# Kernel tuning notes

Hardware: AMD Instinct MI355X
Metric: run time of the kernel (lower is better)

The kernel has to match this reference:

```python
import jax, jax.numpy as jnp
import numpy as np

N, E, D_IN, D_OUT = 100000, 1600000, 128, 128
EPS = 1e-12  # torch F.normalize clamp


def setup_inputs() -> dict:
    key = jax.random.key(0)
    ks = jax.random.split(key, 8)
    return {
        "x": jax.random.normal(ks[0], (N, D_IN), dtype=jnp.float32),
        "edge_src": jax.random.randint(ks[1], (E,), 0, N, dtype=jnp.int32),
        "edge_dst": jax.random.randint(ks[2], (E,), 0, N, dtype=jnp.int32),
        "edge_weight": jax.random.uniform(ks[3], (E,), dtype=jnp.float32),
        "W_l": jax.random.normal(ks[4], (D_IN, D_OUT), dtype=jnp.float32) / np.sqrt(D_IN),
        "b_l": jax.random.normal(ks[5], (D_OUT,), dtype=jnp.float32) * 0.01,
        "W_r": jax.random.normal(ks[6], (D_IN, D_OUT), dtype=jnp.float32) / np.sqrt(D_IN),
        "b_r": jax.random.normal(ks[7], (D_OUT,), dtype=jnp.float32) * 0.01,
    }


def reference(x, edge_src, edge_dst, edge_weight, W_l, b_l, W_r, b_r):
    # spmm(adj, x): weighted gather of source node features, scatter-add to targets
    agg = jax.ops.segment_sum(x[edge_src] * edge_weight[:, None], edge_dst,
                              num_segments=x.shape[0])          # [N, D_IN]
    out = agg @ W_l + b_l + (x @ W_r + b_r)                      # lin_l + lin_r (num_tgt == N)
    # L1 normalize along features (F.normalize, p=1, dim=1)
    l1 = jnp.maximum(jnp.sum(jnp.abs(out), axis=1, keepdims=True), EPS)
    return out / l1
```

## Files before the change

kernel.cpp:

```cpp
#include <hip/hip_runtime.h>
#include <hip/hip_fp16.h>


static constexpr int D = 128;
static constexpr int NB = 1024;
static constexpr int CBITS = 7;
static constexpr int CSZ = 1 << CBITS;
static constexpr int NPART = 256;

typedef _Float16 half8 __attribute__((ext_vector_type(8)));
typedef float f32x4 __attribute__((ext_vector_type(4)));

__global__ __launch_bounds__(256) void cvt_x_fp16(
    const float4* __restrict__ x4, __half2* __restrict__ xh2, int n4)
{
    int i = blockIdx.x * blockDim.x + threadIdx.x;
    int stride = gridDim.x * blockDim.x;
    for (; i < n4; i += stride) {
        float4 v = x4[i];
        xh2[2 * i + 0] = __floats2half2_rn(v.x, v.y);
        xh2[2 * i + 1] = __floats2half2_rn(v.z, v.w);
    }
}

__global__ __launch_bounds__(256) void wt_build(
    const float* __restrict__ Wl, const float* __restrict__ Wr,
    __half* __restrict__ wt)
{
    const int idx = blockIdx.x * blockDim.x + threadIdx.x;
    if (idx >= 128 * 256) return;
    const int c = idx >> 8;
    const int k = idx & 255;
    const float v = (k < 128) ? Wl[(size_t)k * D + c] : Wr[(size_t)(k - 128) * D + c];
    wt[(size_t)c * 256 + k] = __float2half(v);
}

__global__ __launch_bounds__(256) void coarse_count(
    const int* __restrict__ edst, int* __restrict__ bhist, int E, int chunk)
{
    __shared__ int hist[NB];
    for (int t = threadIdx.x; t < NB; t += 256) hist[t] = 0;
    __syncthreads();
    const int beg = blockIdx.x * chunk;
    const int end = min(E, beg + chunk);
    for (int e = beg + threadIdx.x; e < end; e += 256)
        atomicAdd(&hist[edst[e] >> CBITS], 1);
    __syncthreads();
    for (int t = threadIdx.x; t < NB; t += 256)
        bhist[(size_t)blockIdx.x * NB + t] = hist[t];
}

__global__ __launch_bounds__(64) void bucket_scan(
    int* __restrict__ bhist, int* __restrict__ ctot)
{
    const int t = blockIdx.x * 64 + threadIdx.x;
    int run = 0;
    for (int b = 0; b < NPART; b += 8) {
        int v[8];
#pragma unroll
        for (int i = 0; i < 8; ++i)
            v[i] = bhist[(size_t)(b + i) * NB + t];
#pragma unroll
        for (int i = 0; i < 8; ++i) {
            const int c = v[i];
            bhist[(size_t)(b + i) * NB + t] = run;
            run += c;
        }
    }
    ctot[t] = run;
}

__global__ __launch_bounds__(NB) void coarse_scan(
    const int* __restrict__ ctot, int* __restrict__ cbase,
    int* __restrict__ offs, int N, int E)
{
    __shared__ int s[NB];
    const int t = threadIdx.x;
    const int v = ctot[t];
    s[t] = v;
    __syncthreads();
    for (int off = 1; off < NB; off <<= 1) {
        const int u = (t >= off) ? s[t - off] : 0;
        __syncthreads();
        s[t] += u;
        __syncthreads();
    }
    cbase[t] = s[t] - v;
    if (t == NB - 1) { cbase[NB] = s[t]; offs[N] = E; }
}

__global__ __launch_bounds__(256) void coarse_partition(
    const int* __restrict__ esrc, const int* __restrict__ edst,
    const float* __restrict__ ew, const int* __restrict__ bhist,
    const int* __restrict__ cbase,
    int2* __restrict__ cpairs, int E, int chunk)
{
    __shared__ int cur[NB];
    for (int t = threadIdx.x; t < NB; t += 256)
        cur[t] = bhist[(size_t)blockIdx.x * NB + t] + cbase[t];
    __syncthreads();
    const int beg = blockIdx.x * chunk;
    const int end = min(E, beg + chunk);
    for (int e = beg + threadIdx.x; e < end; e += 256) {
        const int d = edst[e];
        const int pos = atomicAdd(&cur[d >> CBITS], 1);
        cpairs[pos] = make_int2(((d & (CSZ - 1)) << 20) | esrc[e],
                                __float_as_int(ew[e]));
    }
}

__global__ __launch_bounds__(256) void fine_sort(
    const int2* __restrict__ cpairs, const int* __restrict__ cbase,
    int* __restrict__ offs, int2* __restrict__ pairs, int N)
{
    __shared__ int hist[CSZ];
    __shared__ int scn[CSZ];
    const int b = blockIdx.x;
    const int t = threadIdx.x;
    const int s0 = cbase[b], s1 = cbase[b + 1];
    if (t < CSZ) hist[t] = 0;
    __syncthreads();
    for (int i = s0 + t; i < s1; i += 256)
        atomicAdd(&hist[(cpairs[i].x >> 20) & (CSZ - 1)], 1);
    __syncthreads();
    if (t < CSZ) scn[t] = hist[t];
    __syncthreads();
    for (int off = 1; off < CSZ; off <<= 1) {
        int u = 0;
        if (t < CSZ && t >= off) u = scn[t - off];
        __syncthreads();
        if (t < CSZ) scn[t] += u;
        __syncthreads();
    }
    if (t < CSZ) {
        const int base = s0 + scn[t] - hist[t];
        const int node = (b << CBITS) + t;
        if (node < N) offs[node] = base;
        hist[t] = base;
    }
    __syncthreads();
    for (int i = s0 + t; i < s1; i += 256) {
        const int2 p = cpairs[i];
        const int pos = atomicAdd(&hist[(p.x >> 20) & (CSZ - 1)], 1);
        pairs[pos] = make_int2(p.x & 0xFFFFF, p.y);
    }
}

template <bool FP16X>
__global__ __launch_bounds__(256) void sage_gather(
    const void* __restrict__ xrows,
    const int2* __restrict__ pairs,
    const int* __restrict__ offs,
    void* __restrict__ agg,
    int N)
{
    int node = (blockIdx.x * blockDim.x + threadIdx.x) >> 6;
    const int lane = threadIdx.x & 63;
    if (node >= N) return;
    node = __builtin_amdgcn_readfirstlane(node);
    const int beg = offs[node];
    const int end = offs[node + 1];
    const int sub = lane >> 5;
    const int cl  = lane & 31;

    const __half* __restrict__ xh = (const __half*)xrows;
    const float*  __restrict__ xf = (const float*)xrows;

    float a0 = 0.f, a1 = 0.f, a2 = 0.f, a3 = 0.f;
    int k = beg;
    for (; k + 8 <= end; k += 8) {
        int s_[4]; float w_[4];
#pragma unroll
        for (int i = 0; i < 4; ++i) {
            const int2 ea = pairs[k + 2 * i + 0];
            const int2 eb = pairs[k + 2 * i + 1];
            s_[i] = sub ? eb.x : ea.x;
            w_[i] = __int_as_float(sub ? eb.y : ea.y);
        }
        if (FP16X) {
            float2 raw[4];
#pragma unroll
            for (int i = 0; i < 4; ++i)
                raw[i] = *reinterpret_cast<const float2*>(&xh[(size_t)s_[i] * D + cl * 4]);
#pragma unroll
            for (int i = 0; i < 4; ++i) {
                union { float2 f2; __half2 h[2]; } u;
                u.f2 = raw[i];
                const float2 f01 = __half22float2(u.h[0]);
                const float2 f23 = __half22float2(u.h[1]);
                a0 = fmaf(f01.x, w_[i], a0);
                a1 = fmaf(f01.y, w_[i], a1);
                a2 = fmaf(f23.x, w_[i], a2);
                a3 = fmaf(f23.y, w_[i], a3);
            }
        } else {
            float4 raw[4];
#pragma unroll
            for (int i = 0; i < 4; ++i)
                raw[i] = *reinterpret_cast<const float4*>(&xf[(size_t)s_[i] * D + cl * 4]);
#pragma unroll
            for (int i = 0; i < 4; ++i) {
                a0 = fmaf(raw[i].x, w_[i], a0);
                a1 = fmaf(raw[i].y, w_[i], a1);
                a2 = fmaf(raw[i].z, w_[i], a2);
                a3 = fmaf(raw[i].w, w_[i], a3);
            }
        }
    }
    for (int t = 0; k + t < end; ++t) {
        if (sub == (t & 1)) {
            const int2 p = pairs[k + t];
            const float w = __int_as_float(p.y);
            if (FP16X) {
                union { float2 f2; __half2 h[2]; } u;
                u.f2 = *reinterpret_cast<const float2*>(&xh[(size_t)p.x * D + cl * 4]);
                const float2 f01 = __half22float2(u.h[0]);
                const float2 f23 = __half22float2(u.h[1]);
                a0 = fmaf(f01.x, w, a0); a1 = fmaf(f01.y, w, a1);
                a2 = fmaf(f23.x, w, a2); a3 = fmaf(f23.y, w, a3);
            } else {
                const float4 v = *reinterpret_cast<const float4*>(&xf[(size_t)p.x * D + cl * 4]);
                a0 = fmaf(v.x, w, a0); a1 = fmaf(v.y, w, a1);
                a2 = fmaf(v.z, w, a2); a3 = fmaf(v.w, w, a3);
            }
        }
    }
    a0 += __shfl_xor(a0, 32, 64);
    a1 += __shfl_xor(a1, 32, 64);
    a2 += __shfl_xor(a2, 32, 64);
    a3 += __shfl_xor(a3, 32, 64);

    if (sub == 0) {
        if (FP16X) {
            union { __half2 h[2]; int2 i2; } u;
            u.h[0] = __floats2half2_rn(a0, a1);
            u.h[1] = __floats2half2_rn(a2, a3);
            *reinterpret_cast<int2*>(&((__half*)agg)[(size_t)node * D + cl * 4]) = u.i2;
        } else {
            *reinterpret_cast<float4*>(&((float*)agg)[(size_t)node * D + cl * 4]) =
                make_float4(a0, a1, a2, a3);
        }
    }
}

__global__ __launch_bounds__(256) void sage_scatter(
    const float* __restrict__ x,
    const int* __restrict__ esrc,
    const int* __restrict__ edst,
    const float* __restrict__ ew,
    float* agg, int E)
{
    const int lane = threadIdx.x & 63;
    const int warp = (blockIdx.x * blockDim.x + threadIdx.x) >> 6;
    const int nwarps = (gridDim.x * blockDim.x) >> 6;
    const float2* __restrict__ x2 = reinterpret_cast<const float2*>(x);
    for (int e = warp; e < E; e += nwarps) {
        const int s = esrc[e];
        const int d = edst[e];
        const float w = ew[e];
        const float2 xv = x2[s * 64 + lane];
        atomicAdd(&agg[d * D + lane * 2 + 0], xv.x * w);
        atomicAdd(&agg[d * D + lane * 2 + 1], xv.y * w);
    }
}

__global__ __launch_bounds__(256) void sage_linear_norm_mfma(
    const __half* __restrict__ aggh,
    const __half* __restrict__ xh,
    const __half* __restrict__ wt,
    const float* __restrict__ bl,
    const float* __restrict__ br,
    float* __restrict__ out,
    int N)
{
    __shared__ __half a_s[64][136];
    __shared__ __half w_s[128][136];
    const int tid = threadIdx.x;
    const int bn = blockIdx.x * 64;
    const int wv = tid >> 6;
    const int l  = tid & 63;
    const int lr = l & 15;
    const int lq = l >> 4;

    f32x4 acc[8];
#pragma unroll
    for (int t = 0; t < 8; ++t) acc[t] = f32x4{0.f, 0.f, 0.f, 0.f};

    const int ar  = tid >> 2;
    const int as  = (tid & 3) * 32;
    const int wr  = tid >> 1;
    const int wsg = (tid & 1) * 64;

#pragma unroll
    for (int c = 0; c < 2; ++c) {
        const __half* __restrict__ A = c ? xh : aggh;
        __syncthreads();
        {
            const int gn = bn + ar;
            half8 v0 = {}, v1 = {}, v2 = {}, v3 = {};
            if (gn < N) {
                const half8* src = reinterpret_cast<const half8*>(&A[(size_t)gn * D + as]);
                v0 = src[0]; v1 = src[1]; v2 = src[2]; v3 = src[3];
            }
            half8* dst = reinterpret_cast<half8*>(&a_s[ar][as]);
            dst[0] = v0; dst[1] = v1; dst[2] = v2; dst[3] = v3;
        }
        {
            const half8* src = reinterpret_cast<const half8*>(&wt[(size_t)wr * 256 + c * 128 + wsg]);
            half8* dst = reinterpret_cast<half8*>(&w_s[wr][wsg]);
#pragma unroll
            for (int j = 0; j < 8; ++j) dst[j] = src[j];
        }
        __syncthreads();

#pragma unroll
        for (int ks = 0; ks < 4; ++ks) {
            const int k0 = ks * 32 + lq * 8;
            const half8 af = *reinterpret_cast<const half8*>(&a_s[wv * 16 + lr][k0]);
#pragma unroll
            for (int t = 0; t < 8; ++t) {
                const half8 bf = *reinterpret_cast<const half8*>(&w_s[t * 16 + lr][k0]);
                acc[t] = __builtin_amdgcn_mfma_f32_16x16x32_f16(af, bf, acc[t], 0, 0, 0);
            }
        }
    }

    float bias[8];
#pragma unroll
    for (int t = 0; t < 8; ++t) {
        const int cidx = t * 16 + lr;
        bias[t] = bl[cidx] + br[cidx];
    }
    float v[8][4];
    float s0 = 0.f, s1 = 0.f, s2 = 0.f, s3 = 0.f;
#pragma unroll
    for (int t = 0; t < 8; ++t) {
        v[t][0] = acc[t][0] + bias[t];
        v[t][1] = acc[t][1] + bias[t];
        v[t][2] = acc[t][2] + bias[t];
        v[t][3] = acc[t][3] + bias[t];
        s0 += fabsf(v[t][0]); s1 += fabsf(v[t][1]);
        s2 += fabsf(v[t][2]); s3 += fabsf(v[t][3]);
    }
#pragma unroll
    for (int m = 1; m < 16; m <<= 1) {
        s0 += __shfl_xor(s0, m, 64);
        s1 += __shfl_xor(s1, m, 64);
        s2 += __shfl_xor(s2, m, 64);
        s3 += __shfl_xor(s3, m, 64);
    }
    const float r0 = 1.0f / fmaxf(s0, 1e-12f);
    const float r1 = 1.0f / fmaxf(s1, 1e-12f);
    const float r2 = 1.0f / fmaxf(s2, 1e-12f);
    const float r3 = 1.0f / fmaxf(s3, 1e-12f);

    const int nd0 = bn + wv * 16 + lq * 4;
#pragma unroll
    for (int r = 0; r < 4; ++r) {
        const int nd = nd0 + r;
        if (nd < N) {
            const float ri = (r == 0) ? r0 : (r == 1) ? r1 : (r == 2) ? r2 : r3;
#pragma unroll
            for (int t = 0; t < 8; ++t)
                out[(size_t)nd * D + t * 16 + lr] = v[t][r] * ri;
        }
    }
}

__global__ __launch_bounds__(256) void sage_linear_norm(
    const float* agg, const float* __restrict__ x,
    const float* __restrict__ Wl, const float* __restrict__ bl,
    const float* __restrict__ Wr, const float* __restrict__ br,
    float* out, int N)
{
    __shared__ float a_s[64][68];
    __shared__ float w_s[64][132];
    const int tid = threadIdx.x;
    const int jg = tid & 31;
    const int ng = tid >> 5;
    const int bn = blockIdx.x * 64;

    float acc[8][4];
#pragma unroll
    for (int i = 0; i < 8; ++i) {
        acc[i][0] = 0.f; acc[i][1] = 0.f; acc[i][2] = 0.f; acc[i][3] = 0.f;
    }
    const int sn  = tid >> 2;
    const int skb = (tid & 3) << 4;
    const int wr  = tid >> 5;
    const int wc  = (tid & 31) << 2;

    for (int c = 0; c < 4; ++c) {
        const float* A = (c < 2) ? agg : x;
        const float* __restrict__ W = (c < 2) ? Wl : Wr;
        const int kb = (c & 1) << 6;
        __syncthreads();
        const int gn = bn + sn;
#pragma unroll
        for (int it = 0; it < 4; ++it) {
            float4 vv = make_float4(0.f, 0.f, 0.f, 0.f);
            if (gn < N)
                vv = *reinterpret_cast<const float4*>(&A[(size_t)gn * D + kb + skb + it * 4]);
            *reinterpret_cast<float4*>(&a_s[sn][skb + it * 4]) = vv;
        }
#pragma unroll
        for (int it = 0; it < 8; ++it) {
            const int row = it * 8 + wr;
            const float4 vv = *reinterpret_cast<const float4*>(&W[(size_t)(kb + row) * D + wc]);
            *reinterpret_cast<float4*>(&w_s[row][wc]) = vv;
        }
        __syncthreads();
#pragma unroll 4
        for (int kk = 0; kk < 64; kk += 4) {
            const float4 w0 = *reinterpret_cast<const float4*>(&w_s[kk + 0][jg << 2]);
            const float4 w1 = *reinterpret_cast<const float4*>(&w_s[kk + 1][jg << 2]);
            const float4 w2 = *reinterpret_cast<const float4*>(&w_s[kk + 2][jg << 2]);
            const float4 w3 = *reinterpret_cast<const float4*>(&w_s[kk + 3][jg << 2]);
#pragma unroll
            for (int i = 0; i < 8; ++i) {
                const float4 av = *reinterpret_cast<const float4*>(&a_s[(ng << 3) + i][kk]);
                acc[i][0] = fmaf(av.w, w3.x, fmaf(av.z, w2.x, fmaf(av.y, w1.x, fmaf(av.x, w0.x, acc[i][0]))));
                acc[i][1] = fmaf(av.w, w3.y, fmaf(av.z, w2.y, fmaf(av.y, w1.y, fmaf(av.x, w0.y, acc[i][1]))));
                acc[i][2] = fmaf(av.w, w3.z, fmaf(av.z, w2.z, fmaf(av.y, w1.z, fmaf(av.x, w0.z, acc[i][2]))));
                acc[i][3] = fmaf(av.w, w3.w, fmaf(av.z, w2.w, fmaf(av.y, w1.w, fmaf(av.x, w0.w, acc[i][3]))));
            }
        }
    }
    const float4 bl4 = *reinterpret_cast<const float4*>(&bl[jg << 2]);
    const float4 br4 = *reinterpret_cast<const float4*>(&br[jg << 2]);
    const float bx = bl4.x + br4.x, by = bl4.y + br4.y,
                bz = bl4.z + br4.z, bw = bl4.w + br4.w;
#pragma unroll
    for (int i = 0; i < 8; ++i) {
        const float v0 = acc[i][0] + bx;
        const float v1 = acc[i][1] + by;
        const float v2 = acc[i][2] + bz;
        const float v3 = acc[i][3] + bw;
        float s = fabsf(v0) + fabsf(v1) + fabsf(v2) + fabsf(v3);
#pragma unroll
        for (int m = 1; m < 32; m <<= 1) s += __shfl_xor(s, m, 64);
        s = fmaxf(s, 1e-12f);
        const float r = 1.0f / s;
        const int n = bn + (ng << 3) + i;
        if (n < N) {
            const float4 o = make_float4(v0 * r, v1 * r, v2 * r, v3 * r);
            *reinterpret_cast<float4*>(&out[(size_t)n * D + (jg << 2)]) = o;
        }
    }
}

extern "C" void kernel_launch(void* const* d_in, const int* in_sizes, int n_in,
                              void* d_out, int out_size, void* d_ws, size_t ws_size,
                              hipStream_t stream) {
    const float* x    = (const float*)d_in[0];
    const int*   esrc = (const int*)  d_in[1];
    const int*   edst = (const int*)  d_in[2];
    const float* ew   = (const float*)d_in[3];
    const float* Wl   = (const float*)d_in[4];
    const float* bl   = (const float*)d_in[5];
    const float* Wr   = (const float*)d_in[6];
    const float* br   = (const float*)d_in[7];
    float* out = (float*)d_out;

    const int N = in_sizes[0] / D;
    const int E = in_sizes[1];

    auto align256 = [](size_t v) { return (v + 255) & ~size_t(255); };
    size_t off_bhist  = 0;
    size_t off_ctot   = align256(off_bhist  + (size_t)NPART * NB * 4);
    size_t off_cbase  = align256(off_ctot   + (size_t)NB * 4);
    size_t off_offs   = align256(off_cbase  + (size_t)(NB + 1) * 4);
    size_t off_cpairs = align256(off_offs   + (size_t)(N + 1) * 4);
    size_t off_pairs  = align256(off_cpairs + (size_t)E * 8);
    size_t off_xh     = align256(off_pairs  + (size_t)E * 8);
    size_t off_aggh   = align256(off_xh     + (size_t)N * D * 2);
    size_t off_wt     = align256(off_aggh   + (size_t)N * D * 2);
    size_t need_b     = off_xh;
    size_t need_a     = off_wt + (size_t)256 * D * 2;

    const bool fits_meta = (N <= (1 << 20)) && ((N + CSZ - 1) >> CBITS) <= NB;

    if (ws_size >= need_b && fits_meta) {
        char* ws = (char*)d_ws;
        int*  bhist  = (int*) (ws + off_bhist);
        int*  ctot   = (int*) (ws + off_ctot);
        int*  cbase  = (int*) (ws + off_cbase);
        int*  offs   = (int*) (ws + off_offs);
        int2* cpairs = (int2*)(ws + off_cpairs);
        int2* pairs  = (int2*)(ws + off_pairs);
        __half2* xh  = (__half2*)(ws + off_xh);
        __half*  agh = (__half*)(ws + off_aggh);
        __half*  wt  = (__half*)(ws + off_wt);

        const bool mfma = (ws_size >= need_a);
        const int chunk = (E + NPART - 1) / NPART;
        const int nbu = (N + CSZ - 1) >> CBITS;

        if (mfma) {
            cvt_x_fp16<<<4096, 256, 0, stream>>>((const float4*)x, xh, N * (D / 4));
            wt_build<<<128, 256, 0, stream>>>(Wl, Wr, wt);
        }
        coarse_count<<<NPART, 256, 0, stream>>>(edst, bhist, E, chunk);
        bucket_scan<<<NB / 64, 64, 0, stream>>>(bhist, ctot);
        coarse_scan<<<1, NB, 0, stream>>>(ctot, cbase, offs, N, E);
        coarse_partition<<<NPART, 256, 0, stream>>>(esrc, edst, ew, bhist, cbase,
                                                    cpairs, E, chunk);
        fine_sort<<<nbu, 256, 0, stream>>>(cpairs, cbase, offs, pairs, N);

        const int gb = (N * 64 + 255) / 256;
        const int nb = (N + 63) / 64;
        if (mfma) {
            sage_gather<true ><<<gb, 256, 0, stream>>>(xh, pairs, offs, agh, N);
            sage_linear_norm_mfma<<<nb, 256, 0, stream>>>(agh, (const __half*)xh, wt,
                                                          bl, br, out, N);
        } else {
            sage_gather<false><<<gb, 256, 0, stream>>>(x, pairs, offs, out, N);
            sage_linear_norm<<<nb, 256, 0, stream>>>(out, x, Wl, bl, Wr, br, out, N);
        }
    } else {
        hipMemsetAsync(out, 0, (size_t)N * D * sizeof(float), stream);
        sage_scatter<<<2048, 256, 0, stream>>>(x, esrc, edst, ew, out, E);
        const int nb = (N + 63) / 64;
        sage_linear_norm<<<nb, 256, 0, stream>>>(out, x, Wl, bl, Wr, br, out, N);
    }
}
```

Measured before the change: 161.0 us.

## Fuse fine sort into bucket gather and merge prep kernels into one launch

Removes the fine_sort kernel and the global pairs/offs arrays. Each gather block now loads its coarse bucket (64 nodes) into shared memory in chunks of up to 2048 edges, does a local counting sort, and aggregates directly from LDS. The fp16 conversion, weight transpose and coarse histogram kernels are merged into a single prep launch. Bucket size halves to 64 nodes with 2048 buckets, and the coarse scan handles two entries per thread. This saves a full global write and read of the sorted edge list plus several launches. In exchange, each block serialises its 64 nodes across 4 waves, and buckets larger than the cap take multiple passes that re-read and re-accumulate into fp16 agg.

```diff
diff --git a/kernel.cpp b/kernel.cpp
--- a/kernel.cpp
+++ b/kernel.cpp
@@ -3,51 +3,56 @@
 
 
 static constexpr int D = 128;
-static constexpr int NB = 1024;
-static constexpr int CBITS = 7;
+static constexpr int CBITS = 6;
 static constexpr int CSZ = 1 << CBITS;
+static constexpr int NB = 2048;
 static constexpr int NPART = 256;
+static constexpr int CAP = 2048;
+static constexpr int PCH = CAP / 256;
 
 typedef _Float16 half8 __attribute__((ext_vector_type(8)));
 typedef float f32x4 __attribute__((ext_vector_type(4)));
 
-__global__ __launch_bounds__(256) void cvt_x_fp16(
-    const float4* __restrict__ x4, __half2* __restrict__ xh2, int n4)
-{
-    int i = blockIdx.x * blockDim.x + threadIdx.x;
-    int stride = gridDim.x * blockDim.x;
-    for (; i < n4; i += stride) {
-        float4 v = x4[i];
-        xh2[2 * i + 0] = __floats2half2_rn(v.x, v.y);
-        xh2[2 * i + 1] = __floats2half2_rn(v.z, v.w);
-    }
-}
-
-__global__ __launch_bounds__(256) void wt_build(
+__global__ __launch_bounds__(256) void prep(
+    const int* __restrict__ edst, int* __restrict__ bhist, int E, int chunk,
+    const float4* __restrict__ x4, __half2* __restrict__ xh2, int n4,
     const float* __restrict__ Wl, const float* __restrict__ Wr,
-    __half* __restrict__ wt)
-{
-    const int idx = blockIdx.x * blockDim.x + threadIdx.x;
-    if (idx >= 128 * 256) return;
-    const int c = idx >> 8;
-    const int k = idx & 255;
-    const float v = (k < 128) ? Wl[(size_t)k * D + c] : Wr[(size_t)(k - 128) * D + c];
-    wt[(size_t)c * 256 + k] = __float2half(v);
-}
-
-__global__ __launch_bounds__(256) void coarse_count(
-    const int* __restrict__ edst, int* __restrict__ bhist, int E, int chunk)
+    __half* __restrict__ wt, int do_cvt)
 {
     __shared__ int hist[NB];
-    for (int t = threadIdx.x; t < NB; t += 256) hist[t] = 0;
-    __syncthreads();
-    const int beg = blockIdx.x * chunk;
-    const int end = min(E, beg + chunk);
-    for (int e = beg + threadIdx.x; e < end; e += 256)
-        atomicAdd(&hist[edst[e] >> CBITS], 1);
-    __syncthreads();
-    for (int t = threadIdx.x; t < NB; t += 256)
-        bhist[(size_t)blockIdx.x * NB + t] = hist[t];
+    const int b = blockIdx.x;
+    const int tid = threadIdx.x;
+    if (b < NPART) {
+        for (int t = tid; t < NB; t += 256) hist[t] = 0;
+        __syncthreads();
+        const int beg = b * chunk;
+        const int end = min(E, beg + chunk);
+        for (int e = beg + tid; e < end; e += 256)
+            atomicAdd(&hist[edst[e] >> CBITS], 1);
+        __syncthreads();
+        for (int t = tid; t < NB; t += 256)
+            bhist[(size_t)b * NB + t] = hist[t];
+    } else if (do_cvt) {
+        const int cb = b - NPART;
+        if (cb < 1024) {
+            int i = cb * 256 + tid;
+            const int stride = 1024 * 256;
+            for (; i < n4; i += stride) {
+                float4 v = x4[i];
+                xh2[2 * i + 0] = __floats2half2_rn(v.x, v.y);
+                xh2[2 * i + 1] = __floats2half2_rn(v.z, v.w);
+            }
+        } else {
+            const int idx = (cb - 1024) * 256 + tid;
+            if (idx < 128 * 256) {
+                const int c = idx >> 8;
+                const int k = idx & 255;
+                const float v = (k < 128) ? Wl[(size_t)k * D + c]
+                                          : Wr[(size_t)(k - 128) * D + c];
+                wt[(size_t)c * 256 + k] = __float2half(v);
+            }
+        }
+    }
 }
 
 __global__ __launch_bounds__(64) void bucket_scan(
@@ -70,23 +75,26 @@
     ctot[t] = run;
 }
 
-__global__ __launch_bounds__(NB) void coarse_scan(
-    const int* __restrict__ ctot, int* __restrict__ cbase,
-    int* __restrict__ offs, int N, int E)
-{
-    __shared__ int s[NB];
+__global__ __launch_bounds__(1024) void coarse_scan(
+    const int* __restrict__ ctot, int* __restrict__ cbase)
+{
+    __shared__ int s[1024];
     const int t = threadIdx.x;
-    const int v = ctot[t];
-    s[t] = v;
+    const int v0 = ctot[2 * t];
+    const int v1 = ctot[2 * t + 1];
+    const int loc = v0 + v1;
+    s[t] = loc;
     __syncthreads();
-    for (int off = 1; off < NB; off <<= 1) {
+    for (int off = 1; off < 1024; off <<= 1) {
         const int u = (t >= off) ? s[t - off] : 0;
         __syncthreads();
         s[t] += u;
         __syncthreads();
     }
-    cbase[t] = s[t] - v;
-    if (t == NB - 1) { cbase[NB] = s[t]; offs[N] = E; }
+    const int excl = s[t] - loc;
+    cbase[2 * t]     = excl;
+    cbase[2 * t + 1] = excl + v0;
+    if (t == 1023) cbase[NB] = s[t];
 }
 
 __global__ __launch_bounds__(256) void coarse_partition(
@@ -109,137 +117,169 @@
     }
 }
 
-__global__ __launch_bounds__(256) void fine_sort(
-    const int2* __restrict__ cpairs, const int* __restrict__ cbase,
-    int* __restrict__ offs, int2* __restrict__ pairs, int N)
-{
-    __shared__ int hist[CSZ];
-    __shared__ int scn[CSZ];
-    const int b = blockIdx.x;
-    const int t = threadIdx.x;
-    const int s0 = cbase[b], s1 = cbase[b + 1];
-    if (t < CSZ) hist[t] = 0;
-    __syncthreads();
-    for (int i = s0 + t; i < s1; i += 256)
-        atomicAdd(&hist[(cpairs[i].x >> 20) & (CSZ - 1)], 1);
-    __syncthreads();
-    if (t < CSZ) scn[t] = hist[t];
-    __syncthreads();
-    for (int off = 1; off < CSZ; off <<= 1) {
-        int u = 0;
-        if (t < CSZ && t >= off) u = scn[t - off];
-        __syncthreads();
-        if (t < CSZ) scn[t] += u;
-        __syncthreads();
-    }
-    if (t < CSZ) {
-        const int base = s0 + scn[t] - hist[t];
-        const int node = (b << CBITS) + t;
-        if (node < N) offs[node] = base;
-        hist[t] = base;
-    }
-    __syncthreads();
-    for (int i = s0 + t; i < s1; i += 256) {
-        const int2 p = cpairs[i];
-        const int pos = atomicAdd(&hist[(p.x >> 20) & (CSZ - 1)], 1);
-        pairs[pos] = make_int2(p.x & 0xFFFFF, p.y);
-    }
-}
-
 template <bool FP16X>
-__global__ __launch_bounds__(256) void sage_gather(
+__global__ __launch_bounds__(256) void bucket_gather(
     const void* __restrict__ xrows,
-    const int2* __restrict__ pairs,
-    const int* __restrict__ offs,
+    const int2* __restrict__ cpairs,
+    const int* __restrict__ cbase,
     void* __restrict__ agg,
     int N)
 {
-    int node = (blockIdx.x * blockDim.x + threadIdx.x) >> 6;
-    const int lane = threadIdx.x & 63;
-    if (node >= N) return;
-    node = __builtin_amdgcn_readfirstlane(node);
-    const int beg = offs[node];
-    const int end = offs[node + 1];
+    __shared__ int2 ep[CAP];
+    __shared__ int hist[CSZ], scn[CSZ], cur[CSZ];
+    const int b   = blockIdx.x;
+    const int tid = threadIdx.x;
+    const int lane = tid & 63;
+    const int wv  = tid >> 6;
     const int sub = lane >> 5;
     const int cl  = lane & 31;
+    const int s0 = cbase[b], s1 = cbase[b + 1];
+    const int nodebase = b << CBITS;
 
     const __half* __restrict__ xh = (const __half*)xrows;
     const float*  __restrict__ xf = (const float*)xrows;
 
-    float a0 = 0.f, a1 = 0.f, a2 = 0.f, a3 = 0.f;
-    int k = beg;
-    for (; k + 8 <= end; k += 8) {
-        int s_[4]; float w_[4];
-#pragma unroll
-        for (int i = 0; i < 4; ++i) {
-            const int2 ea = pairs[k + 2 * i + 0];
-            const int2 eb = pairs[k + 2 * i + 1];
-            s_[i] = sub ? eb.x : ea.x;
-            w_[i] = __int_as_float(sub ? eb.y : ea.y);
-        }
-        if (FP16X) {
-            float2 raw[4];
-#pragma unroll
-            for (int i = 0; i < 4; ++i)
-                raw[i] = *reinterpret_cast<const float2*>(&xh[(size_t)s_[i] * D + cl * 4]);
-#pragma unroll
-            for (int i = 0; i < 4; ++i) {
-                union { float2 f2; __half2 h[2]; } u;
-                u.f2 = raw[i];
-                const float2 f01 = __half22float2(u.h[0]);
-                const float2 f23 = __half22float2(u.h[1]);
-                a0 = fmaf(f01.x, w_[i], a0);
-                a1 = fmaf(f01.y, w_[i], a1);
-                a2 = fmaf(f23.x, w_[i], a2);
-                a3 = fmaf(f23.y, w_[i], a3);
-            }
-        } else {
-            float4 raw[4];
-#pragma unroll
-            for (int i = 0; i < 4; ++i)
-                raw[i] = *reinterpret_cast<const float4*>(&xf[(size_t)s_[i] * D + cl * 4]);
-#pragma unroll
-            for (int i = 0; i < 4; ++i) {
-                a0 = fmaf(raw[i].x, w_[i], a0);
-                a1 = fmaf(raw[i].y, w_[i], a1);
-                a2 = fmaf(raw[i].z, w_[i], a2);
-                a3 = fmaf(raw[i].w, w_[i], a3);
-            }
-        }
-    }
-    for (int t = 0; k + t < end; ++t) {
-        if (sub == (t & 1)) {
-            const int2 p = pairs[k + t];
-            const float w = __int_as_float(p.y);
-            if (FP16X) {
-                union { float2 f2; __half2 h[2]; } u;
-                u.f2 = *reinterpret_cast<const float2*>(&xh[(size_t)p.x * D + cl * 4]);
-                const float2 f01 = __half22float2(u.h[0]);
-                const float2 f23 = __half22float2(u.h[1]);
-                a0 = fmaf(f01.x, w, a0); a1 = fmaf(f01.y, w, a1);
-                a2 = fmaf(f23.x, w, a2); a3 = fmaf(f23.y, w, a3);
-            } else {
-                const float4 v = *reinterpret_cast<const float4*>(&xf[(size_t)p.x * D + cl * 4]);
-                a0 = fmaf(v.x, w, a0); a1 = fmaf(v.y, w, a1);
-                a2 = fmaf(v.z, w, a2); a3 = fmaf(v.w, w, a3);
-            }
-        }
-    }
-    a0 += __shfl_xor(a0, 32, 64);
-    a1 += __shfl_xor(a1, 32, 64);
-    a2 += __shfl_xor(a2, 32, 64);
-    a3 += __shfl_xor(a3, 32, 64);
-
-    if (sub == 0) {
-        if (FP16X) {
-            union { __half2 h[2]; int2 i2; } u;
-            u.h[0] = __floats2half2_rn(a0, a1);
-            u.h[1] = __floats2half2_rn(a2, a3);
-            *reinterpret_cast<int2*>(&((__half*)agg)[(size_t)node * D + cl * 4]) = u.i2;
-        } else {
-            *reinterpret_cast<float4*>(&((float*)agg)[(size_t)node * D + cl * 4]) =
-                make_float4(a0, a1, a2, a3);
-        }
+    int t0 = s0;
+    bool first = true;
+    while (true) {
+        const int t1 = min(s1, t0 + CAP);
+
+        if (tid < CSZ) hist[tid] = 0;
+        __syncthreads();
+        int2 pc[PCH];
+#pragma unroll
+        for (int j = 0; j < PCH; ++j) {
+            const int i = t0 + tid + j * 256;
+            if (i < t1) {
+                const int2 p = cpairs[i];
+                pc[j] = p;
+                atomicAdd(&hist[(p.x >> 20) & (CSZ - 1)], 1);
+            }
+        }
+        __syncthreads();
+        if (tid < CSZ) {
+            const int v = hist[tid];
+            int xs = v;
+#pragma unroll
+            for (int off = 1; off < 64; off <<= 1) {
+                const int y = __shfl_up(xs, off, 64);
+                if (lane >= off) xs += y;
+            }
+            scn[tid] = xs - v;
+            cur[tid] = xs - v;
+        }
+        __syncthreads();
+#pragma unroll
+        for (int j = 0; j < PCH; ++j) {
+            const int i = t0 + tid + j * 256;
+            if (i < t1) {
+                const int2 p = pc[j];
+                const int pos = atomicAdd(&cur[(p.x >> 20) & (CSZ - 1)], 1);
+                ep[pos] = make_int2(p.x & 0xFFFFF, p.y);
+            }
+        }
+        __syncthreads();
+
+        for (int i = 0; i < CSZ / 4; ++i) {
+            const int ln = wv * (CSZ / 4) + i;
+            int node = nodebase + ln;
+            if (node >= N) break;
+            node = __builtin_amdgcn_readfirstlane(node);
+            const int lo = scn[ln];
+            const int hi = lo + hist[ln];
+
+            float a0 = 0.f, a1 = 0.f, a2 = 0.f, a3 = 0.f;
+            int k = lo;
+            for (; k + 8 <= hi; k += 8) {
+                const int2 p0 = ep[k + 0 + sub];
+                const int2 p1 = ep[k + 2 + sub];
+                const int2 p2 = ep[k + 4 + sub];
+                const int2 p3 = ep[k + 6 + sub];
+                const int   s_[4] = { p0.x, p1.x, p2.x, p3.x };
+                const float w_[4] = { __int_as_float(p0.y), __int_as_float(p1.y),
+                                      __int_as_float(p2.y), __int_as_float(p3.y) };
+                if (FP16X) {
+                    float2 raw[4];
+#pragma unroll
+                    for (int q = 0; q < 4; ++q)
+                        raw[q] = *reinterpret_cast<const float2*>(&xh[(size_t)s_[q] * D + cl * 4]);
+#pragma unroll
+                    for (int q = 0; q < 4; ++q) {
+                        union { float2 f2; __half2 h[2]; } u;
+                        u.f2 = raw[q];
+                        const float2 f01 = __half22float2(u.h[0]);
+                        const float2 f23 = __half22float2(u.h[1]);
+                        a0 = fmaf(f01.x, w_[q], a0);
+                        a1 = fmaf(f01.y, w_[q], a1);
+                        a2 = fmaf(f23.x, w_[q], a2);
+                        a3 = fmaf(f23.y, w_[q], a3);
+                    }
+                } else {
+                    float4 raw[4];
+#pragma unroll
+                    for (int q = 0; q < 4; ++q)
+                        raw[q] = *reinterpret_cast<const float4*>(&xf[(size_t)s_[q] * D + cl * 4]);
+#pragma unroll
+                    for (int q = 0; q < 4; ++q) {
+                        a0 = fmaf(raw[q].x, w_[q], a0);
+                        a1 = fmaf(raw[q].y, w_[q], a1);
+                        a2 = fmaf(raw[q].z, w_[q], a2);
+                        a3 = fmaf(raw[q].w, w_[q], a3);
+                    }
+                }
+            }
+            for (int t = 0; k + t < hi; ++t) {
+                if (sub == (t & 1)) {
+                    const int2 p = ep[k + t];
+                    const float w = __int_as_float(p.y);
+                    if (FP16X) {
+                        union { float2 f2; __half2 h[2]; } u;
+                        u.f2 = *reinterpret_cast<const float2*>(&xh[(size_t)p.x * D + cl * 4]);
+                        const float2 f01 = __half22float2(u.h[0]);
+                        const float2 f23 = __half22float2(u.h[1]);
+                        a0 = fmaf(f01.x, w, a0); a1 = fmaf(f01.y, w, a1);
+                        a2 = fmaf(f23.x, w, a2); a3 = fmaf(f23.y, w, a3);
+                    } else {
+                        const float4 v = *reinterpret_cast<const float4*>(&xf[(size_t)p.x * D + cl * 4]);
+                        a0 = fmaf(v.x, w, a0); a1 = fmaf(v.y, w, a1);
+                        a2 = fmaf(v.z, w, a2); a3 = fmaf(v.w, w, a3);
+                    }
+                }
+            }
+            a0 += __shfl_xor(a0, 32, 64);
+            a1 += __shfl_xor(a1, 32, 64);
+            a2 += __shfl_xor(a2, 32, 64);
+            a3 += __shfl_xor(a3, 32, 64);
+
+            if (sub == 0) {
+                if (FP16X) {
+                    __half* ap = &((__half*)agg)[(size_t)node * D + cl * 4];
+                    if (!first) {
+                        union { int2 i2; __half2 h[2]; } o;
+                        o.i2 = *reinterpret_cast<int2*>(ap);
+                        const float2 e01 = __half22float2(o.h[0]);
+                        const float2 e23 = __half22float2(o.h[1]);
+                        a0 += e01.x; a1 += e01.y; a2 += e23.x; a3 += e23.y;
+                    }
+                    union { __half2 h[2]; int2 i2; } u;
+                    u.h[0] = __floats2half2_rn(a0, a1);
+                    u.h[1] = __floats2half2_rn(a2, a3);
+                    *reinterpret_cast<int2*>(ap) = u.i2;
+                } else {
+                    float* ap = &((float*)agg)[(size_t)node * D + cl * 4];
+                    if (!first) {
+                        const float4 e = *reinterpret_cast<float4*>(ap);
+                        a0 += e.x; a1 += e.y; a2 += e.z; a3 += e.w;
+                    }
+                    *reinterpret_cast<float4*>(ap) = make_float4(a0, a1, a2, a3);
+                }
+            }
+        }
+
+        t0 = t1;
+        first = false;
+        if (t0 >= s1) break;
+        __syncthreads();
     }
 }
 
@@ -469,52 +509,45 @@
     size_t off_bhist  = 0;
     size_t off_ctot   = align256(off_bhist  + (size_t)NPART * NB * 4);
     size_t off_cbase  = align256(off_ctot   + (size_t)NB * 4);
-    size_t off_offs   = align256(off_cbase  + (size_t)(NB + 1) * 4);
-    size_t off_cpairs = align256(off_offs   + (size_t)(N + 1) * 4);
-    size_t off_pairs  = align256(off_cpairs + (size_t)E * 8);
-    size_t off_xh     = align256(off_pairs  + (size_t)E * 8);
+    size_t off_cpairs = align256(off_cbase  + (size_t)(NB + 1) * 4);
+    size_t off_xh     = align256(off_cpairs + (size_t)E * 8);
     size_t off_aggh   = align256(off_xh     + (size_t)N * D * 2);
     size_t off_wt     = align256(off_aggh   + (size_t)N * D * 2);
     size_t need_b     = off_xh;
     size_t need_a     = off_wt + (size_t)256 * D * 2;
 
-    const bool fits_meta = (N <= (1 << 20)) && ((N + CSZ - 1) >> CBITS) <= NB;
+    const int nbu = (N + CSZ - 1) >> CBITS;
+    const bool fits_meta = (N <= (1 << 20)) && (nbu <= NB);
 
     if (ws_size >= need_b && fits_meta) {
         char* ws = (char*)d_ws;
         int*  bhist  = (int*) (ws + off_bhist);
         int*  ctot   = (int*) (ws + off_ctot);
         int*  cbase  = (int*) (ws + off_cbase);
-        int*  offs   = (int*) (ws + off_offs);
         int2* cpairs = (int2*)(ws + off_cpairs);
-        int2* pairs  = (int2*)(ws + off_pairs);
         __half2* xh  = (__half2*)(ws + off_xh);
         __half*  agh = (__half*)(ws + off_aggh);
         __half*  wt  = (__half*)(ws + off_wt);
 
         const bool mfma = (ws_size >= need_a);
         const int chunk = (E + NPART - 1) / NPART;
-        const int nbu = (N + CSZ - 1) >> CBITS;
-
-        if (mfma) {
-            cvt_x_fp16<<<4096, 256, 0, stream>>>((const float4*)x, xh, N * (D / 4));
-            wt_build<<<128, 256, 0, stream>>>(Wl, Wr, wt);
-        }
-        coarse_count<<<NPART, 256, 0, stream>>>(edst, bhist, E, chunk);
+
+        const int prep_grid = NPART + (mfma ? (1024 + 128) : 0);
+        prep<<<prep_grid, 256, 0, stream>>>(edst, bhist, E, chunk,
+                                            (const float4*)x, xh, N * (D / 4),
+                                            Wl, Wr, wt, mfma ? 1 : 0);
         bucket_scan<<<NB / 64, 64, 0, stream>>>(bhist, ctot);
-        coarse_scan<<<1, NB, 0, stream>>>(ctot, cbase, offs, N, E);
+        coarse_scan<<<1, 1024, 0, stream>>>(ctot, cbase);
         coarse_partition<<<NPART, 256, 0, stream>>>(esrc, edst, ew, bhist, cbase,
                                                     cpairs, E, chunk);
-        fine_sort<<<nbu, 256, 0, stream>>>(cpairs, cbase, offs, pairs, N);
-
-        const int gb = (N * 64 + 255) / 256;
+
         const int nb = (N + 63) / 64;
         if (mfma) {
-            sage_gather<true ><<<gb, 256, 0, stream>>>(xh, pairs, offs, agh, N);
+            bucket_gather<true ><<<nbu, 256, 0, stream>>>(xh, cpairs, cbase, agh, N);
             sage_linear_norm_mfma<<<nb, 256, 0, stream>>>(agh, (const __half*)xh, wt,
                                                           bl, br, out, N);
         } else {
-            sage_gather<false><<<gb, 256, 0, stream>>>(x, pairs, offs, out, N);
+            bucket_gather<false><<<nbu, 256, 0, stream>>>(x, cpairs, cbase, out, N);
             sage_linear_norm<<<nb, 256, 0, stream>>>(out, x, Wl, bl, Wr, br, out, N);
         }
     } else {
```

After: 173.1 us. 7.5% more time.

## Merge preprocessing kernels, use finer coarse buckets, unroll partition loops

Applied to the files above, without the earlier changes.

Fuses the x fp16 conversion, weight transpose and destination histogram into one launch, so three kernel launches become one and the independent work runs concurrently. It halves the coarse bucket width (64 nodes, 2048 buckets), so the fine sort has smaller per-block segments and can replace its shared-memory scan with a single-wavefront shuffle scan. The count and partition loops are unrolled by four to keep more loads in flight. In exchange, the histogram and bucket-offset buffers double in size, bucket_scan gets more work, and coarse_scan now handles two entries per thread.

```diff
diff --git a/kernel.cpp b/kernel.cpp
--- a/kernel.cpp
+++ b/kernel.cpp
@@ -3,51 +3,65 @@
 
 
 static constexpr int D = 128;
-static constexpr int NB = 1024;
-static constexpr int CBITS = 7;
+static constexpr int CBITS = 6;
 static constexpr int CSZ = 1 << CBITS;
+static constexpr int NB = 2048;
 static constexpr int NPART = 256;
 
 typedef _Float16 half8 __attribute__((ext_vector_type(8)));
 typedef float f32x4 __attribute__((ext_vector_type(4)));
 
-__global__ __launch_bounds__(256) void cvt_x_fp16(
-    const float4* __restrict__ x4, __half2* __restrict__ xh2, int n4)
-{
-    int i = blockIdx.x * blockDim.x + threadIdx.x;
-    int stride = gridDim.x * blockDim.x;
-    for (; i < n4; i += stride) {
-        float4 v = x4[i];
-        xh2[2 * i + 0] = __floats2half2_rn(v.x, v.y);
-        xh2[2 * i + 1] = __floats2half2_rn(v.z, v.w);
-    }
-}
-
-__global__ __launch_bounds__(256) void wt_build(
+__global__ __launch_bounds__(256) void prep(
+    const int* __restrict__ edst, int* __restrict__ bhist, int E, int chunk,
+    const float4* __restrict__ x4, __half2* __restrict__ xh2, int n4,
     const float* __restrict__ Wl, const float* __restrict__ Wr,
-    __half* __restrict__ wt)
-{
-    const int idx = blockIdx.x * blockDim.x + threadIdx.x;
-    if (idx >= 128 * 256) return;
-    const int c = idx >> 8;
-    const int k = idx & 255;
-    const float v = (k < 128) ? Wl[(size_t)k * D + c] : Wr[(size_t)(k - 128) * D + c];
-    wt[(size_t)c * 256 + k] = __float2half(v);
-}
-
-__global__ __launch_bounds__(256) void coarse_count(
-    const int* __restrict__ edst, int* __restrict__ bhist, int E, int chunk)
+    __half* __restrict__ wt, int do_cvt)
 {
     __shared__ int hist[NB];
-    for (int t = threadIdx.x; t < NB; t += 256) hist[t] = 0;
-    __syncthreads();
-    const int beg = blockIdx.x * chunk;
-    const int end = min(E, beg + chunk);
-    for (int e = beg + threadIdx.x; e < end; e += 256)
-        atomicAdd(&hist[edst[e] >> CBITS], 1);
-    __syncthreads();
-    for (int t = threadIdx.x; t < NB; t += 256)
-        bhist[(size_t)blockIdx.x * NB + t] = hist[t];
+    const int b = blockIdx.x;
+    const int tid = threadIdx.x;
+    if (b < NPART) {
+        for (int t = tid; t < NB; t += 256) hist[t] = 0;
+        __syncthreads();
+        const int beg = b * chunk;
+        const int end = min(E, beg + chunk);
+        int e = beg + tid;
+        for (; e + 3 * 256 < end; e += 4 * 256) {
+            const int d0 = edst[e];
+            const int d1 = edst[e + 256];
+            const int d2 = edst[e + 512];
+            const int d3 = edst[e + 768];
+            atomicAdd(&hist[d0 >> CBITS], 1);
+            atomicAdd(&hist[d1 >> CBITS], 1);
+            atomicAdd(&hist[d2 >> CBITS], 1);
+            atomicAdd(&hist[d3 >> CBITS], 1);
+        }
+        for (; e < end; e += 256)
+            atomicAdd(&hist[edst[e] >> CBITS], 1);
+        __syncthreads();
+        for (int t = tid; t < NB; t += 256)
+            bhist[(size_t)b * NB + t] = hist[t];
+    } else if (do_cvt) {
+        const int cb = b - NPART;
+        if (cb < 1024) {
+            int i = cb * 256 + tid;
+            const int stride = 1024 * 256;
+            for (; i < n4; i += stride) {
+                float4 v = x4[i];
+                xh2[2 * i + 0] = __floats2half2_rn(v.x, v.y);
+                xh2[2 * i + 1] = __floats2half2_rn(v.z, v.w);
+            }
+        } else {
+            const int idx = (cb - 1024) * 256 + tid;
+            if (idx < 128 * 256) {
+                const int c = idx >> 8;
+                const int k = idx & 255;
+                const float v = (k < 128) ? Wl[(size_t)k * D + c]
+                                          : Wr[(size_t)(k - 128) * D + c];
+                wt[(size_t)c * 256 + k] = __float2half(v);
+            }
+        }
+    }
 }
 
 __global__ __launch_bounds__(64) void bucket_scan(
@@ -70,23 +84,27 @@
     ctot[t] = run;
 }
 
-__global__ __launch_bounds__(NB) void coarse_scan(
+__global__ __launch_bounds__(1024) void coarse_scan(
     const int* __restrict__ ctot, int* __restrict__ cbase,
     int* __restrict__ offs, int N, int E)
 {
-    __shared__ int s[NB];
+    __shared__ int s[1024];
     const int t = threadIdx.x;
-    const int v = ctot[t];
-    s[t] = v;
+    const int v0 = ctot[2 * t];
+    const int v1 = ctot[2 * t + 1];
+    const int loc = v0 + v1;
+    s[t] = loc;
     __syncthreads();
-    for (int off = 1; off < NB; off <<= 1) {
+    for (int off = 1; off < 1024; off <<= 1) {
         const int u = (t >= off) ? s[t - off] : 0;
         __syncthreads();
         s[t] += u;
         __syncthreads();
     }
-    cbase[t] = s[t] - v;
-    if (t == NB - 1) { cbase[NB] = s[t]; offs[N] = E; }
+    const int excl = s[t] - loc;
+    cbase[2 * t]     = excl;
+    cbase[2 * t + 1] = excl + v0;
+    if (t == 1023) { cbase[NB] = s[t]; offs[N] = E; }
 }
 
 __global__ __launch_bounds__(256) void coarse_partition(
@@ -101,7 +119,23 @@
     __syncthreads();
     const int beg = blockIdx.x * chunk;
     const int end = min(E, beg + chunk);
-    for (int e = beg + threadIdx.x; e < end; e += 256) {
+    int e = beg + threadIdx.x;
+    for (; e + 3 * 256 < end; e += 4 * 256) {
+        int d_[4], s_[4]; float w_[4];
+#pragma unroll
+        for (int i = 0; i < 4; ++i) {
+            d_[i] = edst[e + i * 256];
+            s_[i] = esrc[e + i * 256];
+            w_[i] = ew[e + i * 256];
+        }
+#pragma unroll
+        for (int i = 0; i < 4; ++i) {
+            const int pos = atomicAdd(&cur[d_[i] >> CBITS], 1);
+            cpairs[pos] = make_int2(((d_[i] & (CSZ - 1)) << 20) | s_[i],
+                                    __float_as_int(w_[i]));
+        }
+    }
+    for (; e < end; e += 256) {
         const int d = edst[e];
         const int pos = atomicAdd(&cur[d >> CBITS], 1);
         cpairs[pos] = make_int2(((d & (CSZ - 1)) << 20) | esrc[e],
@@ -113,35 +147,34 @@
     const int2* __restrict__ cpairs, const int* __restrict__ cbase,
     int* __restrict__ offs, int2* __restrict__ pairs, int N)
 {
-    __shared__ int hist[CSZ];
-    __shared__ int scn[CSZ];
+    __shared__ int hist[CSZ], scn[CSZ], cur[CSZ];
     const int b = blockIdx.x;
     const int t = threadIdx.x;
+    const int lane = t & 63;
     const int s0 = cbase[b], s1 = cbase[b + 1];
     if (t < CSZ) hist[t] = 0;
     __syncthreads();
     for (int i = s0 + t; i < s1; i += 256)
         atomicAdd(&hist[(cpairs[i].x >> 20) & (CSZ - 1)], 1);
     __syncthreads();
-    if (t < CSZ) scn[t] = hist[t];
-    __syncthreads();
-    for (int off = 1; off < CSZ; off <<= 1) {
-        int u = 0;
-        if (t < CSZ && t >= off) u = scn[t - off];
-        __syncthreads();
-        if (t < CSZ) scn[t] += u;
-        __syncthreads();
-    }
     if (t < CSZ) {
-        const int base = s0 + scn[t] - hist[t];
+        const int v = hist[t];
+        int xs = v;
+#pragma unroll
+        for (int off = 1; off < 64; off <<= 1) {
+            const int y = __shfl_up(xs, off, 64);
+            if (lane >= off) xs += y;
+        }
+        const int base = s0 + xs - v;
+        scn[t] = base;
+        cur[t] = base;
         const int node = (b << CBITS) + t;
         if (node < N) offs[node] = base;
-        hist[t] = base;
     }
     __syncthreads();
     for (int i = s0 + t; i < s1; i += 256) {
         const int2 p = cpairs[i];
-        const int pos = atomicAdd(&hist[(p.x >> 20) & (CSZ - 1)], 1);
+        const int pos = atomicAdd(&cur[(p.x >> 20) & (CSZ - 1)], 1);
         pairs[pos] = make_int2(p.x & 0xFFFFF, p.y);
     }
 }
@@ -478,7 +511,8 @@
     size_t need_b     = off_xh;
     size_t need_a     = off_wt + (size_t)256 * D * 2;
 
-    const bool fits_meta = (N <= (1 << 20)) && ((N + CSZ - 1) >> CBITS) <= NB;
+    const int nbu = (N + CSZ - 1) >> CBITS;
+    const bool fits_meta = (N <= (1 << 20)) && (nbu <= NB);
 
     if (ws_size >= need_b && fits_meta) {
         char* ws = (char*)d_ws;
@@ -494,15 +528,13 @@
 
         const bool mfma = (ws_size >= need_a);
         const int chunk = (E + NPART - 1) / NPART;
-        const int nbu = (N + CSZ - 1) >> CBITS;
-
-        if (mfma) {
-            cvt_x_fp16<<<4096, 256, 0, stream>>>((const float4*)x, xh, N * (D / 4));
-            wt_build<<<128, 256, 0, stream>>>(Wl, Wr, wt);
-        }
-        coarse_count<<<NPART, 256, 0, stream>>>(edst, bhist, E, chunk);
+
+        const int prep_grid = NPART + (mfma ? (1024 + 128) : 0);
+        prep<<<prep_grid, 256, 0, stream>>>(edst, bhist, E, chunk,
+                                            (const float4*)x, xh, N * (D / 4),
+                                            Wl, Wr, wt, mfma ? 1 : 0);
         bucket_scan<<<NB / 64, 64, 0, stream>>>(bhist, ctot);
-        coarse_scan<<<1, NB, 0, stream>>>(ctot, cbase, offs, N, E);
+        coarse_scan<<<1, 1024, 0, stream>>>(ctot, cbase, offs, N, E);
         coarse_partition<<<NPART, 256, 0, stream>>>(esrc, edst, ew, bhist, cbase,
                                                     cpairs, E, chunk);
         fine_sort<<<nbu, 256, 0, stream>>>(cpairs, cbase, offs, pairs, N);
```

Result: faster. 149.3 us (-7.3%).
